# Optimization experiments

Measured on AMD Instinct MI355X. Metric: run time of the kernel, lower is better.

The kernel has to match this reference:

```python
import jax, jax.numpy as jnp
import numpy as np

N_NODES = 20000
N_EDGES = 320000
NODE_DIM = 512
HIDDEN = 512
N_GRAPHS = 64


def setup_inputs() -> dict:
    key = jax.random.key(0)
    ks = jax.random.split(key, 12)
    s = 0.02
    return {
        "joint_x": jax.random.normal(ks[0], (N_NODES, NODE_DIM), jnp.float32),
        "joint_edge_index": jax.random.randint(ks[1], (2, N_EDGES), 0, N_NODES, dtype=jnp.int32),
        "joint_batch": jnp.sort(jax.random.randint(ks[2], (N_NODES,), 0, N_GRAPHS, dtype=jnp.int32)),
        "W_g1": jax.random.normal(ks[3], (NODE_DIM, HIDDEN), jnp.float32) * s,
        "b_g1": jnp.zeros((HIDDEN,), jnp.float32),
        "W_g2": jax.random.normal(ks[4], (HIDDEN, HIDDEN), jnp.float32) * s,
        "b_g2": jnp.zeros((HIDDEN,), jnp.float32),
        "W_c1": jax.random.normal(ks[5], (HIDDEN, HIDDEN // 2), jnp.float32) * s,
        "b_c1": jnp.zeros((HIDDEN // 2,), jnp.float32),
        "W_c2": jax.random.normal(ks[6], (HIDDEN // 2, 1), jnp.float32) * s,
        "b_c2": jnp.zeros((1,), jnp.float32),
    }


def _gin_layer(h, src, dst, W, b):
    # GINConv(nn=Linear, eps=0): nn((1+eps)*x_i + sum_{j->i} x_j)
    agg = jax.ops.segment_sum(h[src], dst, num_segments=N_NODES)  # [N, D]
    return (h + agg) @ W + b


def reference(joint_x, joint_edge_index, joint_batch, W_g1, b_g1, W_g2, b_g2, W_c1, b_c1, W_c2, b_c2):
    src, dst = joint_edge_index[0], joint_edge_index[1]
    h = _gin_layer(joint_x, src, dst, W_g1, b_g1)  # [N, HIDDEN]
    h = _gin_layer(h, src, dst, W_g2, b_g2)        # [N, HIDDEN]
    pooled = jax.ops.segment_sum(h, joint_batch, num_segments=N_GRAPHS)  # [G, HIDDEN]
    z = jax.nn.relu(pooled @ W_c1 + b_c1)
    score = z @ W_c2 + b_c2                        # [G, 1]
    return jax.nn.sigmoid(score).squeeze(-1)       # [G]
```

## Files before the change

kernel.cpp:

```cpp
#include <hip/hip_runtime.h>
#include <math.h>

constexpr int N_NODES = 20000;
constexpr int DIM = 512;
constexpr int NG = 64;
constexpr int CAP = 64;
constexpr int KCH = 80;
constexpr int NCHUNK = (N_NODES + KCH - 1) / KCH;
constexpr int NSPLIT = 2;
constexpr int RSPLIT = 10;
constexpr int CPS = (NCHUNK + RSPLIT - 1) / RSPLIT;
constexpr int CGS = 32;
constexpr int CSTR = 16;
constexpr int NODE_BLOCKS = (N_NODES + 3) / 4;
constexpr int INIT_BLOCKS = (N_NODES + 255) / 256;
constexpr int GEMM_TILES = 17 * 4;
constexpr int KSPLIT_TILES = GEMM_TILES * 2;
constexpr int PQ_ELEMS = 513 * 256;
constexpr int EPT = 2;
constexpr int EDGE_BLOCKS = (320000 + 256 * EPT - 1) / (256 * EPT);

__device__ __forceinline__ int lower_bound_i(const int* __restrict__ a, int n, int v) {
  int lo = 0, hi = n;
  while (lo < hi) {
    int mid = (lo + hi) >> 1;
    if (a[mid] < v) lo = mid + 1; else hi = mid;
  }
  return lo;
}

__global__ __launch_bounds__(256) void node_init(const int* __restrict__ batch,
                                                 int* __restrict__ cursor,
                                                 float* __restrict__ ng,
                                                 float* __restrict__ cgpad, int n_nodes) {
  int node = blockIdx.x * 256 + threadIdx.x;
  if (node < n_nodes) cursor[(size_t)node * CSTR] = 0;
  if (blockIdx.x == 0 && threadIdx.x < 64) {
    int gg = threadIdx.x;
    int s0 = lower_bound_i(batch, n_nodes, gg);
    int e0 = lower_bound_i(batch, n_nodes, gg + 1);
    ng[gg] = (float)(e0 - s0);
    cgpad[gg * CGS] = 0.f;
  }
}

__device__ void gemm_stack_tile(const float* __restrict__ A0, const float* __restrict__ extra,
                                const float* __restrict__ B, const float* __restrict__ B2,
                                float* __restrict__ C,
                                int N, int K, int R0, int tile, int kbeg, int kend,
                                float* As, float* Bs, int tid) {
  int bm = (tile >> 2) * 32;
  int bn = (tile & 3) * 64;
  int tx = tid & 15;
  int ty = tid >> 4;
  int ar = tid >> 3;
  int ac = (tid & 7) * 2;
  int br = tid >> 4;
  int bc = (tid & 15) * 4;
  float acc[2][4] = {};
  for (int k0 = kbeg; k0 < kend; k0 += 16) {
    int row = bm + ar;
    float2 av = make_float2(0.f, 0.f);
    if (row < R0)       av = *(const float2*)(A0 + (size_t)row * K + k0 + ac);
    else if (row == R0) av = *(const float2*)(extra + k0 + ac);
    As[(ac + 0) * 34 + ar] = av.x;
    As[(ac + 1) * 34 + ar] = av.y;
    size_t boff = (size_t)(k0 + br) * N + bn + bc;
    float4 bv = *(const float4*)(B + boff);
    if (B2) {
      float4 b2 = *(const float4*)(B2 + boff);
      bv.x += b2.x; bv.y += b2.y; bv.z += b2.z; bv.w += b2.w;
    }
    *(float4*)&Bs[br * 68 + bc] = bv;
    __syncthreads();
#pragma unroll
    for (int kk = 0; kk < 16; ++kk) {
      float2 a01 = *(const float2*)&As[kk * 34 + ty * 2];
      float4 b4  = *(const float4*)&Bs[kk * 68 + tx * 4];
      acc[0][0] = fmaf(a01.x, b4.x, acc[0][0]); acc[0][1] = fmaf(a01.x, b4.y, acc[0][1]);
      acc[0][2] = fmaf(a01.x, b4.z, acc[0][2]); acc[0][3] = fmaf(a01.x, b4.w, acc[0][3]);
      acc[1][0] = fmaf(a01.y, b4.x, acc[1][0]); acc[1][1] = fmaf(a01.y, b4.y, acc[1][1]);
      acc[1][2] = fmaf(a01.y, b4.z, acc[1][2]); acc[1][3] = fmaf(a01.y, b4.w, acc[1][3]);
    }
    __syncthreads();
  }
#pragma unroll
  for (int i = 0; i < 2; ++i) {
    int m = bm + ty * 2 + i;
    if (m > R0) continue;
    *(float4*)&C[(size_t)m * N + bn + tx * 4] =
        make_float4(acc[i][0], acc[i][1], acc[i][2], acc[i][3]);
  }
}

__global__ __launch_bounds__(256) void fill_and_Q(const int* __restrict__ srcI,
                                                  const int* __restrict__ dstI,
                                                  const int* __restrict__ batch,
                                                  int* __restrict__ cursor,
                                                  int* __restrict__ edst,
                                                  float* __restrict__ cgpad,
                                                  const float* __restrict__ Wg2,
                                                  const float* __restrict__ bg2,
                                                  const float* __restrict__ Wc1,
                                                  float* __restrict__ Q, int n_edges) {
  __shared__ float As[16 * 34];
  __shared__ float Bs[16 * 68];
  __shared__ int hist[64];
  int b = blockIdx.x;
  int t = threadIdx.x;
  if (b < KSPLIT_TILES) {
    int ks = b & 1;
    int tile = b >> 1;
    gemm_stack_tile(Wg2, bg2, Wc1, nullptr, Q + (size_t)ks * PQ_ELEMS,
                    256, 512, 512, tile, ks * 256, ks * 256 + 256, As, Bs, t);
  } else {
    int eb = b - KSPLIT_TILES;
    if (t < 64) hist[t] = 0;
    __syncthreads();
    int base = eb * (256 * EPT) + t;
    int s[EPT], d[EPT], c[EPT];
    bool v[EPT];
#pragma unroll
    for (int u = 0; u < EPT; ++u) {
      int i = base + u * 256;
      v[u] = i < n_edges;
      s[u] = v[u] ? srcI[i] : 0;
    }
#pragma unroll
    for (int u = 0; u < EPT; ++u) {
      int i = base + u * 256;
      d[u] = v[u] ? dstI[i] : 0;
    }
#pragma unroll
    for (int u = 0; u < EPT; ++u)
      if (v[u]) c[u] = atomicAdd(&cursor[(size_t)s[u] * CSTR], 1);
#pragma unroll
    for (int u = 0; u < EPT; ++u)
      if (v[u]) edst[(size_t)s[u] * CAP + c[u]] = d[u];
#pragma unroll
    for (int u = 0; u < EPT; ++u)
      if (v[u]) atomicAdd(&hist[batch[d[u]]], 1);
    __syncthreads();
    if (t < 64 && hist[t] != 0) atomicAdd(&cgpad[t * CGS], (float)hist[t]);
  }
}

__global__ __launch_bounds__(256) void build_wT(const int* __restrict__ batch,
                                                const int* __restrict__ deg,
                                                const int* __restrict__ edst,
                                                float* __restrict__ wT, int n_nodes) {
  int node = blockIdx.x * 4 + (threadIdx.x >> 6);
  int g = threadIdx.x & 63;
  if (node >= n_nodes) return;
  int end = deg[(size_t)node * CSTR];
  const int* nb = edst + (size_t)node * CAP;
  float acc = (batch[node] == g) ? 1.f : 0.f;
  int i = 0;
  for (; i + 7 < end; i += 8) {
    int d0 = nb[i], d1 = nb[i + 1], d2 = nb[i + 2], d3 = nb[i + 3];
    int d4 = nb[i + 4], d5 = nb[i + 5], d6 = nb[i + 6], d7 = nb[i + 7];
    int b0 = batch[d0], b1 = batch[d1], b2 = batch[d2], b3 = batch[d3];
    int b4 = batch[d4], b5 = batch[d5], b6 = batch[d6], b7 = batch[d7];
    acc += ((float)(b0 == g) + (float)(b1 == g)) + ((float)(b2 == g) + (float)(b3 == g)) +
           ((float)(b4 == g) + (float)(b5 == g)) + ((float)(b6 == g) + (float)(b7 == g));
  }
  for (; i < end; ++i) acc += (float)(batch[nb[i]] == g);
  wT[(size_t)node * 64 + g] = acc;
}

__global__ __launch_bounds__(256) void cT_and_P(const float* __restrict__ wT,
                                                const int* __restrict__ deg,
                                                const int* __restrict__ edst,
                                                float* __restrict__ cT,
                                                const float* __restrict__ Wg1,
                                                const float* __restrict__ bg1,
                                                const float* __restrict__ Q,
                                                float* __restrict__ P, int n_nodes) {
  __shared__ float As[16 * 34];
  __shared__ float Bs[16 * 68];
  int b = blockIdx.x;
  int t = threadIdx.x;
  if (b < KSPLIT_TILES) {
    int ks = b & 1;
    int tile = b >> 1;
    gemm_stack_tile(Wg1, bg1, Q, Q + PQ_ELEMS, P + (size_t)ks * PQ_ELEMS,
                    256, 512, 512, tile, ks * 256, ks * 256 + 256, As, Bs, t);
  } else {
    int node = (b - KSPLIT_TILES) * 4 + (t >> 6);
    int g = t & 63;
    if (node >= n_nodes) return;
    float acc = wT[(size_t)node * 64 + g];
    int end = deg[(size_t)node * CSTR];
    const int* nb = edst + (size_t)node * CAP;
    int i = 0;
    for (; i + 7 < end; i += 8) {
      int d0 = nb[i], d1 = nb[i + 1], d2 = nb[i + 2], d3 = nb[i + 3];
      int d4 = nb[i + 4], d5 = nb[i + 5], d6 = nb[i + 6], d7 = nb[i + 7];
      float v0 = wT[(size_t)d0 * 64 + g], v1 = wT[(size_t)d1 * 64 + g];
      float v2 = wT[(size_t)d2 * 64 + g], v3 = wT[(size_t)d3 * 64 + g];
      float v4 = wT[(size_t)d4 * 64 + g], v5 = wT[(size_t)d5 * 64 + g];
      float v6 = wT[(size_t)d6 * 64 + g], v7 = wT[(size_t)d7 * 64 + g];
      acc += ((v0 + v1) + (v2 + v3)) + ((v4 + v5) + (v6 + v7));
    }
    for (; i + 3 < end; i += 4) {
      int d0 = nb[i], d1 = nb[i + 1], d2 = nb[i + 2], d3 = nb[i + 3];
      acc += wT[(size_t)d0 * 64 + g] + wT[(size_t)d1 * 64 + g] +
             wT[(size_t)d2 * 64 + g] + wT[(size_t)d3 * 64 + g];
    }
    for (; i < end; ++i) acc += wT[(size_t)nb[i] * 64 + g];
    cT[(size_t)node * 64 + g] = acc;
  }
}

#define LOADX(X, KB)                                                      \
  _Pragma("unroll")                                                       \
  for (int t_ = 0; t_ < 4; ++t_) {                                        \
    X[t_][0] = x2[(size_t)(k0 + (KB) + t_) * 256 + ncol];                 \
    X[t_][1] = x2[(size_t)(k0 + (KB) + t_) * 256 + ncol + 64];            \
  }

#define COMPX(X, KB)                                                      \
  _Pragma("unroll")                                                       \
  for (int t_ = 0; t_ < 4; ++t_) {                                        \
    const float4* cp_ = (const float4*)&scT[(KB) + t_][w * 8];            \
    float4 cA_ = cp_[0], cB_ = cp_[1];                                    \
    float cv_[8] = {cA_.x, cA_.y, cA_.z, cA_.w, cB_.x, cB_.y, cB_.z, cB_.w}; \
    _Pragma("unroll")                                                     \
    for (int q_ = 0; q_ < 8; ++q_) {                                      \
      acc[q_][0].x = fmaf(cv_[q_], X[t_][0].x, acc[q_][0].x);             \
      acc[q_][0].y = fmaf(cv_[q_], X[t_][0].y, acc[q_][0].y);             \
      acc[q_][1].x = fmaf(cv_[q_], X[t_][1].x, acc[q_][1].x);             \
      acc[q_][1].y = fmaf(cv_[q_], X[t_][1].y, acc[q_][1].y);             \
    }                                                                     \
  }

__global__ __launch_bounds__(512, 4) void ugemm(const float* __restrict__ x,
                                                const float* __restrict__ cT,
                                                float* __restrict__ Upart, int n_nodes) {
  __shared__ float scT[KCH][64];
  int c = blockIdx.y;
  int nx = blockIdx.x;
  int t = threadIdx.x;
  int w = t >> 6;
  int g = t & 63;
  int k0 = c * KCH;
  int kmax = (n_nodes - k0) < KCH ? (n_nodes - k0) : KCH;
  {
    const float4* src = (const float4*)(cT + (size_t)k0 * 64);
    float4* dst = (float4*)(&scT[0][0]);
    int limit4 = kmax * 16;
    for (int i = t; i < limit4; i += 512) dst[i] = src[i];
  }
  __syncthreads();
  const float2* x2 = (const float2*)x;
  int ncol = nx * 128 + g;
  float2 acc[8][2];
#pragma unroll
  for (int q = 0; q < 8; ++q) {
    acc[q][0] = make_float2(0.f, 0.f);
    acc[q][1] = make_float2(0.f, 0.f);
  }
  float2 xa[4][2], xb[4][2];
  LOADX(xa, 0);
  for (int kk = 0; kk < kmax; kk += 8) {
    LOADX(xb, kk + 4);
    COMPX(xa, kk);
    if (kk + 8 < kmax) { LOADX(xa, kk + 8); }
    COMPX(xb, kk + 4);
  }
  float2* up = (float2*)Upart;
#pragma unroll
  for (int q = 0; q < 8; ++q) {
    int gg = w * 8 + q;
    up[((size_t)c * 64 + gg) * 256 + ncol] = acc[q][0];
    up[((size_t)c * 64 + gg) * 256 + ncol + 64] = acc[q][1];
  }
}

__global__ __launch_bounds__(128) void reduce_U(const float* __restrict__ Upart,
                                                float* __restrict__ Ured) {
  int g = blockIdx.x;
  int s = blockIdx.y;
  int t = threadIdx.x;
  int c0 = s * CPS;
  int c1 = (c0 + CPS < NCHUNK) ? c0 + CPS : NCHUNK;
  const float4* up = (const float4*)Upart;
  float4 acc = make_float4(0.f, 0.f, 0.f, 0.f);
  for (int c = c0; c < c1; ++c) {
    float4 v = up[((size_t)c * 64 + g) * 128 + t];
    acc.x += v.x; acc.y += v.y; acc.z += v.z; acc.w += v.w;
  }
  ((float4*)Ured)[((size_t)s * 64 + g) * 128 + t] = acc;
}

__global__ __launch_bounds__(256) void head(const float* __restrict__ Ured,
                                            const float* __restrict__ P,
                                            const float* __restrict__ Q,
                                            const float* __restrict__ ng,
                                            const float* __restrict__ cgpad,
                                            const float* __restrict__ bc1,
                                            const float* __restrict__ Wc2,
                                            const float* __restrict__ bc2,
                                            float* __restrict__ out) {
  int g = blockIdx.x;
  int j = threadIdx.x;
  const float* Wc0 = P;
  const float* Wc1p = P + (size_t)PQ_ELEMS;
  const float* v1a = P + (size_t)512 * 256;
  const float* v1b = P + (size_t)PQ_ELEMS + (size_t)512 * 256;
  const float* v2a = Q + (size_t)512 * 256;
  const float* v2b = Q + (size_t)PQ_ELEMS + (size_t)512 * 256;
  __shared__ float p[512];
  float s0 = 0.f, s1 = 0.f;
#pragma unroll
  for (int s = 0; s < RSPLIT; ++s) {
    s0 += Ured[((size_t)s * 64 + g) * DIM + j];
    s1 += Ured[((size_t)s * 64 + g) * DIM + 256 + j];
  }
  p[j] = s0;
  p[j + 256] = s1;
  __syncthreads();
  float cg = ng[g] + cgpad[g * CGS];
  float acc = bc1[j] + cg * (v1a[j] + v1b[j]) + ng[g] * (v2a[j] + v2b[j]);
  for (int k = 0; k < 512; ++k) {
    float w = Wc0[k * 256 + j] + Wc1p[k * 256 + j];
    acc = fmaf(p[k], w, acc);
  }
  float z = fmaxf(acc, 0.f);
  float part = z * Wc2[j];
  for (int off = 32; off > 0; off >>= 1) part += __shfl_down(part, off, 64);
  __shared__ float red[4];
  if ((j & 63) == 0) red[j >> 6] = part;
  __syncthreads();
  if (j == 0) {
    float tot = red[0] + red[1] + red[2] + red[3] + bc2[0];
    out[g] = 1.f / (1.f + expf(-tot));
  }
}

extern "C" void kernel_launch(void* const* d_in, const int* in_sizes, int n_in,
                              void* d_out, int out_size, void* d_ws, size_t ws_size,
                              hipStream_t stream) {
  const float* x    = (const float*)d_in[0];
  const int*   ei   = (const int*)d_in[1];
  const int*   batch= (const int*)d_in[2];
  const float* Wg1  = (const float*)d_in[3];
  const float* bg1  = (const float*)d_in[4];
  const float* Wg2  = (const float*)d_in[5];
  const float* bg2  = (const float*)d_in[6];
  const float* Wc1  = (const float*)d_in[7];
  const float* bc1  = (const float*)d_in[8];
  const float* Wc2  = (const float*)d_in[9];
  const float* bc2  = (const float*)d_in[10];
  float* out = (float*)d_out;

  int n_edges = in_sizes[1] / 2;
  int n_nodes = in_sizes[2];
  const int* srcI = ei;
  const int* dstI = ei + n_edges;

  char* ws = (char*)d_ws;
  size_t off = 0;
  auto alloc = [&](size_t bytes) { char* p = ws + off; off += (bytes + 255) & ~(size_t)255; return p; };
  float* wT    = (float*)alloc((size_t)N_NODES * 64 * sizeof(float));
  float* cT    = (float*)alloc((size_t)N_NODES * 64 * sizeof(float));
  float* Upart = (float*)alloc((size_t)NCHUNK * 64 * DIM * sizeof(float));
  float* Ured  = (float*)alloc((size_t)RSPLIT * 64 * DIM * sizeof(float));
  float* Q     = (float*)alloc((size_t)2 * PQ_ELEMS * sizeof(float));
  float* P     = (float*)alloc((size_t)2 * PQ_ELEMS * sizeof(float));
  float* ng    = (float*)alloc(NG * sizeof(float));
  float* cgpad = (float*)alloc(NG * CGS * sizeof(float));
  int* cursor  = (int*)alloc((size_t)N_NODES * CSTR * sizeof(int));
  int* edst    = (int*)alloc((size_t)N_NODES * CAP * sizeof(int));

  node_init<<<INIT_BLOCKS, 256, 0, stream>>>(batch, cursor, ng, cgpad, n_nodes);
  fill_and_Q<<<KSPLIT_TILES + EDGE_BLOCKS, 256, 0, stream>>>(srcI, dstI, batch, cursor, edst,
                                                             cgpad, Wg2, bg2, Wc1, Q, n_edges);
  build_wT<<<NODE_BLOCKS, 256, 0, stream>>>(batch, cursor, edst, wT, n_nodes);
  cT_and_P<<<KSPLIT_TILES + NODE_BLOCKS, 256, 0, stream>>>(wT, cursor, edst, cT,
                                                           Wg1, bg1, Q, P, n_nodes);
  ugemm<<<dim3(NSPLIT, NCHUNK), 512, 0, stream>>>(x, cT, Upart, n_nodes);
  reduce_U<<<dim3(64, RSPLIT), 128, 0, stream>>>(Upart, Ured);
  head<<<NG, 256, 0, stream>>>(Ured, P, Q, ng, cgpad, bc1, Wc2, bc2, out);
}
```

Baseline: 223.2 us.

## Store wT/cT in fp16 and retile ugemm to narrower columns, larger K chunks

The per-node graph-count matrices wT and cT are now stored as half precision, halving their memory traffic in the gather and in ugemm's shared-memory fill, where values are widened back to float. ugemm now has each thread handle one float2 column instead of two, with four column splits instead of two. K chunks double to 160 rows, which halves the number of partial U blocks and the reduce work, and occupancy hints drop to 3. Integer counts are exact in fp16, but cT sums could lose precision if they exceed 2048. The larger shared tile and smaller per-thread work change the occupancy and reuse balance.

New measurement: 218.9 us. About the same (-1.9%).

```diff
diff --git a/kernel.cpp b/kernel.cpp
--- a/kernel.cpp
+++ b/kernel.cpp
@@ -1,14 +1,15 @@
 #include <hip/hip_runtime.h>
+#include <hip/hip_fp16.h>
 #include <math.h>
 
 constexpr int N_NODES = 20000;
 constexpr int DIM = 512;
 constexpr int NG = 64;
 constexpr int CAP = 64;
-constexpr int KCH = 80;
+constexpr int KCH = 160;
 constexpr int NCHUNK = (N_NODES + KCH - 1) / KCH;
-constexpr int NSPLIT = 2;
-constexpr int RSPLIT = 10;
+constexpr int NSPLIT = 4;
+constexpr int RSPLIT = 5;
 constexpr int CPS = (NCHUNK + RSPLIT - 1) / RSPLIT;
 constexpr int CGS = 32;
 constexpr int CSTR = 16;
@@ -148,7 +149,7 @@
 __global__ __launch_bounds__(256) void build_wT(const int* __restrict__ batch,
                                                 const int* __restrict__ deg,
                                                 const int* __restrict__ edst,
-                                                float* __restrict__ wT, int n_nodes) {
+                                                __half* __restrict__ wT, int n_nodes) {
   int node = blockIdx.x * 4 + (threadIdx.x >> 6);
   int g = threadIdx.x & 63;
   if (node >= n_nodes) return;
@@ -165,13 +166,13 @@
            ((float)(b4 == g) + (float)(b5 == g)) + ((float)(b6 == g) + (float)(b7 == g));
   }
   for (; i < end; ++i) acc += (float)(batch[nb[i]] == g);
-  wT[(size_t)node * 64 + g] = acc;
-}
-
-__global__ __launch_bounds__(256) void cT_and_P(const float* __restrict__ wT,
+  wT[(size_t)node * 64 + g] = __float2half_rn(acc);
+}
+
+__global__ __launch_bounds__(256) void cT_and_P(const __half* __restrict__ wT,
                                                 const int* __restrict__ deg,
                                                 const int* __restrict__ edst,
-                                                float* __restrict__ cT,
+                                                __half* __restrict__ cT,
                                                 const float* __restrict__ Wg1,
                                                 const float* __restrict__ bg1,
                                                 const float* __restrict__ Q,
@@ -189,34 +190,37 @@
     int node = (b - KSPLIT_TILES) * 4 + (t >> 6);
     int g = t & 63;
     if (node >= n_nodes) return;
-    float acc = wT[(size_t)node * 64 + g];
+    float acc = __half2float(wT[(size_t)node * 64 + g]);
     int end = deg[(size_t)node * CSTR];
     const int* nb = edst + (size_t)node * CAP;
     int i = 0;
     for (; i + 7 < end; i += 8) {
       int d0 = nb[i], d1 = nb[i + 1], d2 = nb[i + 2], d3 = nb[i + 3];
       int d4 = nb[i + 4], d5 = nb[i + 5], d6 = nb[i + 6], d7 = nb[i + 7];
-      float v0 = wT[(size_t)d0 * 64 + g], v1 = wT[(size_t)d1 * 64 + g];
-      float v2 = wT[(size_t)d2 * 64 + g], v3 = wT[(size_t)d3 * 64 + g];
-      float v4 = wT[(size_t)d4 * 64 + g], v5 = wT[(size_t)d5 * 64 + g];
-      float v6 = wT[(size_t)d6 * 64 + g], v7 = wT[(size_t)d7 * 64 + g];
+      float v0 = __half2float(wT[(size_t)d0 * 64 + g]);
+      float v1 = __half2float(wT[(size_t)d1 * 64 + g]);
+      float v2 = __half2float(wT[(size_t)d2 * 64 + g]);
+      float v3 = __half2float(wT[(size_t)d3 * 64 + g]);
+      float v4 = __half2float(wT[(size_t)d4 * 64 + g]);
+      float v5 = __half2float(wT[(size_t)d5 * 64 + g]);
+      float v6 = __half2float(wT[(size_t)d6 * 64 + g]);
+      float v7 = __half2float(wT[(size_t)d7 * 64 + g]);
       acc += ((v0 + v1) + (v2 + v3)) + ((v4 + v5) + (v6 + v7));
     }
     for (; i + 3 < end; i += 4) {
       int d0 = nb[i], d1 = nb[i + 1], d2 = nb[i + 2], d3 = nb[i + 3];
-      acc += wT[(size_t)d0 * 64 + g] + wT[(size_t)d1 * 64 + g] +
-             wT[(size_t)d2 * 64 + g] + wT[(size_t)d3 * 64 + g];
-    }
-    for (; i < end; ++i) acc += wT[(size_t)nb[i] * 64 + g];
-    cT[(size_t)node * 64 + g] = acc;
+      acc += __half2float(wT[(size_t)d0 * 64 + g]) + __half2float(wT[(size_t)d1 * 64 + g]) +
+             __half2float(wT[(size_t)d2 * 64 + g]) + __half2float(wT[(size_t)d3 * 64 + g]);
+    }
+    for (; i < end; ++i) acc += __half2float(wT[(size_t)nb[i] * 64 + g]);
+    cT[(size_t)node * 64 + g] = __float2half_rn(acc);
   }
 }
 
 #define LOADX(X, KB)                                                      \
   _Pragma("unroll")                                                       \
   for (int t_ = 0; t_ < 4; ++t_) {                                        \
-    X[t_][0] = x2[(size_t)(k0 + (KB) + t_) * 256 + ncol];                 \
-    X[t_][1] = x2[(size_t)(k0 + (KB) + t_) * 256 + ncol + 64];            \
+    X[t_] = x2[(size_t)(k0 + (KB) + t_) * 256 + ncol];                    \
   }
 
 #define COMPX(X, KB)                                                      \
@@ -227,15 +231,13 @@
     float cv_[8] = {cA_.x, cA_.y, cA_.z, cA_.w, cB_.x, cB_.y, cB_.z, cB_.w}; \
     _Pragma("unroll")                                                     \
     for (int q_ = 0; q_ < 8; ++q_) {                                      \
-      acc[q_][0].x = fmaf(cv_[q_], X[t_][0].x, acc[q_][0].x);             \
-      acc[q_][0].y = fmaf(cv_[q_], X[t_][0].y, acc[q_][0].y);             \
-      acc[q_][1].x = fmaf(cv_[q_], X[t_][1].x, acc[q_][1].x);             \
-      acc[q_][1].y = fmaf(cv_[q_], X[t_][1].y, acc[q_][1].y);             \
+      acc[q_].x = fmaf(cv_[q_], X[t_].x, acc[q_].x);                      \
+      acc[q_].y = fmaf(cv_[q_], X[t_].y, acc[q_].y);                      \
     }                                                                     \
   }
 
-__global__ __launch_bounds__(512, 4) void ugemm(const float* __restrict__ x,
-                                                const float* __restrict__ cT,
+__global__ __launch_bounds__(512, 3) void ugemm(const float* __restrict__ x,
+                                                const __half* __restrict__ cT,
                                                 float* __restrict__ Upart, int n_nodes) {
   __shared__ float scT[KCH][64];
   int c = blockIdx.y;
@@ -246,21 +248,25 @@
   int k0 = c * KCH;
   int kmax = (n_nodes - k0) < KCH ? (n_nodes - k0) : KCH;
   {
-    const float4* src = (const float4*)(cT + (size_t)k0 * 64);
-    float4* dst = (float4*)(&scT[0][0]);
+    const uint2* src = (const uint2*)(cT + (size_t)k0 * 64);
+    float4* dstf = (float4*)(&scT[0][0]);
     int limit4 = kmax * 16;
-    for (int i = t; i < limit4; i += 512) dst[i] = src[i];
+    for (int i = t; i < limit4; i += 512) {
+      uint2 v = src[i];
+      __half2 h0 = *(__half2*)&v.x;
+      __half2 h1 = *(__half2*)&v.y;
+      float2 f0 = __half22float2(h0);
+      float2 f1 = __half22float2(h1);
+      dstf[i] = make_float4(f0.x, f0.y, f1.x, f1.y);
+    }
   }
   __syncthreads();
   const float2* x2 = (const float2*)x;
-  int ncol = nx * 128 + g;
-  float2 acc[8][2];
-#pragma unroll
-  for (int q = 0; q < 8; ++q) {
-    acc[q][0] = make_float2(0.f, 0.f);
-    acc[q][1] = make_float2(0.f, 0.f);
-  }
-  float2 xa[4][2], xb[4][2];
+  int ncol = nx * 64 + g;
+  float2 acc[8];
+#pragma unroll
+  for (int q = 0; q < 8; ++q) acc[q] = make_float2(0.f, 0.f);
+  float2 xa[4], xb[4];
   LOADX(xa, 0);
   for (int kk = 0; kk < kmax; kk += 8) {
     LOADX(xb, kk + 4);
@@ -272,8 +278,7 @@
 #pragma unroll
   for (int q = 0; q < 8; ++q) {
     int gg = w * 8 + q;
-    up[((size_t)c * 64 + gg) * 256 + ncol] = acc[q][0];
-    up[((size_t)c * 64 + gg) * 256 + ncol + 64] = acc[q][1];
+    up[((size_t)c * 64 + gg) * 256 + ncol] = acc[q];
   }
 }
 
@@ -362,8 +367,8 @@
   char* ws = (char*)d_ws;
   size_t off = 0;
   auto alloc = [&](size_t bytes) { char* p = ws + off; off += (bytes + 255) & ~(size_t)255; return p; };
-  float* wT    = (float*)alloc((size_t)N_NODES * 64 * sizeof(float));
-  float* cT    = (float*)alloc((size_t)N_NODES * 64 * sizeof(float));
+  __half* wT   = (__half*)alloc((size_t)N_NODES * 64 * sizeof(__half));
+  __half* cT   = (__half*)alloc((size_t)N_NODES * 64 * sizeof(__half));
   float* Upart = (float*)alloc((size_t)NCHUNK * 64 * DIM * sizeof(float));
   float* Ured  = (float*)alloc((size_t)RSPLIT * 64 * DIM * sizeof(float));
   float* Q     = (float*)alloc((size_t)2 * PQ_ELEMS * sizeof(float));
```
